# Optimization experiments

Measured on AMD Instinct MI355X. Metric: run time of the kernel, lower is better.

## Reference

```python
import jax, jax.numpy as jnp
import numpy as np

EPS = 1e-3  # denominator regularizer for weighted mean/cov
DIST_SCALE = 10.0  # raw_call applies 10.0 * distsq before exp weighting

V, K, C, F = 100000, 40, 3, 32


def setup_inputs() -> dict:
    key = jax.random.key(0)
    k1, k2, k3, k4 = jax.random.split(key, 4)
    coordinates = jax.random.normal(k1, (V, C), dtype=jnp.float32)
    distsq = jax.random.uniform(k2, (V, K), dtype=jnp.float32)  # squared distances >= 0
    features = jax.random.uniform(k3, (V, F), dtype=jnp.float32)  # non-negative activations
    n_idxs = jax.random.randint(k4, (V, K), 0, V, dtype=jnp.int32)
    return {"coordinates": coordinates, "distsq": distsq, "features": features, "n_idxs": n_idxs}


def reference(coordinates, distsq, features, n_idxs):
    nV, nC = coordinates.shape
    nF = features.shape[1]
    # SelectWithDefault semantics: index -1 -> default 0
    valid = (n_idxs >= 0)
    idx = jnp.where(valid, n_idxs, 0)
    n_coords = jnp.where(valid[..., None], coordinates[idx], 0.0)  # V x K x C
    w = jnp.exp(-DIST_SCALE * distsq)  # V x K distance weights
    n_feat = jnp.where(valid[..., None], features[idx], 0.0) * w[..., None]  # V x K x F (feature weights)
    wsum = jnp.sum(n_feat, axis=1)  # V x F
    denom = wsum[:, :, None] + EPS  # V x F x 1
    # weighted first moment -> means, weighted second moment -> covariance
    means = jnp.einsum('vkf,vkc->vfc', n_feat, n_coords) / denom  # V x F x C
    second = jnp.einsum('vkf,vkc,vkd->vfcd', n_feat, n_coords, n_coords) / denom[..., None]  # V x F x C x C
    cov = second - means[:, :, :, None] * means[:, :, None, :]  # centered covariance
    out = jnp.concatenate([cov.reshape(nV, nF * nC * nC), means.reshape(nV, nF * nC)], axis=-1)
    return out
```

## Files before the change

kernel.cpp:

```cpp
#include <hip/hip_runtime.h>


constexpr int K = 40;
constexpr int C = 3;
constexpr int F = 32;
constexpr float EPS = 1e-3f;
constexpr float DIST_SCALE = 10.0f;
constexpr int OUT_PER_V = F * C * C + F * C;
constexpr int VPB = 16;
constexpr int PAIRS = VPB * K;
constexpr int STAGE_F4 = VPB * 48;

typedef float    floatx4 __attribute__((ext_vector_type(4)));
typedef float    f32x8   __attribute__((ext_vector_type(8)));
typedef _Float16 f16x8   __attribute__((ext_vector_type(8)));

__global__ __launch_bounds__(256) void cvt_kernel(
    const float* __restrict__ in, _Float16* __restrict__ out16, int n8)
{
    const int i = blockIdx.x * 256 + threadIdx.x;
    if (i < n8) {
        const f32x8 v = __builtin_nontemporal_load((const f32x8*)in + i);
        const f16x8 o = __builtin_convertvector(v, f16x8);
        *((f16x8*)out16 + i) = o;
    }
}

template <typename FT>
__global__ __launch_bounds__(256) void neighcov_kernel(
    const float* __restrict__ coords,
    const float* __restrict__ distsq,
    const FT*    __restrict__ features,
    const int*   __restrict__ nidx,
    float* __restrict__ out,
    int V)
{
    __shared__ float4  s_wxyz[PAIRS];
    __shared__ int     s_joff[PAIRS];
    __shared__ floatx4 s_stage[STAGE_F4];

    const int tid   = threadIdx.x;
    const int vbase = blockIdx.x * VPB;
    const long long total_pairs = (long long)V * K;

    #pragma unroll
    for (int p = tid; p < PAIRS; p += 256) {
        const long long gp = (long long)vbase * K + p;
        int idx = -1;
        float d = 0.f;
        if (gp < total_pairs) {
            idx = __builtin_nontemporal_load(nidx + gp);
            d   = __builtin_nontemporal_load(distsq + gp);
        }
        const bool valid = (idx >= 0);
        const int j = valid ? idx : 0;
        const float w = valid ? __expf(-DIST_SCALE * d) : 0.f;
        const float x = coords[(size_t)j * 3 + 0];
        const float y = coords[(size_t)j * 3 + 1];
        const float z = coords[(size_t)j * 3 + 2];
        s_wxyz[p] = make_float4(w, x, y, z);
        s_joff[p] = j * F;
    }
    __syncthreads();

    const int fl   = tid & 15;
    const int vloc = tid >> 4;
    const float4* wp = &s_wxyz[vloc * K];
    const int*    jp = &s_joff[vloc * K];
    const int rem_v = V - vbase;
    floatx4* o4 = (floatx4*)(out + (size_t)vbase * OUT_PER_V);

    #pragma unroll
    for (int half = 0; half < 2; ++half) {
        const int f = half * 16 + fl;

        float wsum = 0.f;
        float m0 = 0.f, m1 = 0.f, m2 = 0.f;
        float s00 = 0.f, s01 = 0.f, s02 = 0.f, s11 = 0.f, s12 = 0.f, s22 = 0.f;

        #pragma unroll 8
        for (int k = 0; k < K; ++k) {
            const float4 q = wp[k];
            const int jo   = jp[k];
            const float feat = (float)features[jo + f];
            const float fw = q.x * feat;
            const float x = q.y, y = q.z, z = q.w;
            const float fx = fw * x, fy = fw * y, fz = fw * z;
            wsum += fw;
            m0 += fx;        m1 += fy;        m2 += fz;
            s00 += fx * x;   s01 += fx * y;   s02 += fx * z;
            s11 += fy * y;   s12 += fy * z;   s22 += fz * z;
        }

        const float inv = 1.f / (wsum + EPS);
        const float mu0 = m0 * inv, mu1 = m1 * inv, mu2 = m2 * inv;
        const float c00 = s00 * inv - mu0 * mu0;
        const float c01 = s01 * inv - mu0 * mu1;
        const float c02 = s02 * inv - mu0 * mu2;
        const float c11 = s11 * inv - mu1 * mu1;
        const float c12 = s12 * inv - mu1 * mu2;
        const float c22 = s22 * inv - mu2 * mu2;

        float* s_out = (float*)s_stage;
        float* so = s_out + vloc * 192 + fl * 9;
        so[0] = c00; so[1] = c01; so[2] = c02;
        so[3] = c01; so[4] = c11; so[5] = c12;
        so[6] = c02; so[7] = c12; so[8] = c22;
        float* sm = s_out + vloc * 192 + 144 + fl * 3;
        sm[0] = mu0; sm[1] = mu1; sm[2] = mu2;

        __syncthreads();

        #pragma unroll
        for (int g = tid; g < STAGE_F4; g += 256) {
            const int v = g / 48;
            const int r = g - v * 48;
            if (v < rem_v) {
                const int dst = v * 96 + (r < 36 ? half * 36 + r
                                                 : 72 + half * 12 + (r - 36));
                __builtin_nontemporal_store(s_stage[g], o4 + dst);
            }
        }

        __syncthreads();
    }
}

extern "C" void kernel_launch(void* const* d_in, const int* in_sizes, int n_in,
                              void* d_out, int out_size, void* d_ws, size_t ws_size,
                              hipStream_t stream) {
    const float* coords   = (const float*)d_in[0];
    const float* distsq   = (const float*)d_in[1];
    const float* features = (const float*)d_in[2];
    const int*   nidx     = (const int*)d_in[3];
    float* out = (float*)d_out;

    const int V = in_sizes[0] / C;
    const int blocks = (V + VPB - 1) / VPB;

    const size_t need = (size_t)V * F * sizeof(_Float16);
    const int nelem = V * F;
    if (ws_size >= need && (nelem & 7) == 0) {
        _Float16* feat16 = (_Float16*)d_ws;
        const int n8 = nelem / 8;
        cvt_kernel<<<(n8 + 255) / 256, 256, 0, stream>>>(features, feat16, n8);
        neighcov_kernel<_Float16><<<blocks, 256, 0, stream>>>(
            coords, distsq, feat16, nidx, out, V);
    } else {
        neighcov_kernel<float><<<blocks, 256, 0, stream>>>(
            coords, distsq, features, nidx, out, V);
    }
}
```

Measured before the change: 271.7 us.

## Split fp16 features into low/high half planes and pad shared weight array

The conversion kernel now writes features into two separate fp16 planes, one per 16-feature half. Each half-pass of the main kernel gathers from a compact 32-byte row instead of part of a 64-byte row, which aims to improve cache-line use for the random neighbor gathers. The shared weight/coordinate array is padded to stride K+1 to change the bank mapping, and the fp32 fallback is rewritten with 8 vertices per block. The trade-off is that each neighbor row is now touched twice, in two different planes, across the two passes.

```diff
diff --git a/kernel.cpp b/kernel.cpp
--- a/kernel.cpp
+++ b/kernel.cpp
@@ -4,11 +4,13 @@
 constexpr int K = 40;
 constexpr int C = 3;
 constexpr int F = 32;
+constexpr int FH = 16;
 constexpr float EPS = 1e-3f;
 constexpr float DIST_SCALE = 10.0f;
 constexpr int OUT_PER_V = F * C * C + F * C;
 constexpr int VPB = 16;
 constexpr int PAIRS = VPB * K;
+constexpr int WSTRIDE = K + 1;
 constexpr int STAGE_F4 = VPB * 48;
 
 typedef float    floatx4 __attribute__((ext_vector_type(4)));
@@ -16,26 +18,28 @@
 typedef _Float16 f16x8   __attribute__((ext_vector_type(8)));
 
 __global__ __launch_bounds__(256) void cvt_kernel(
-    const float* __restrict__ in, _Float16* __restrict__ out16, int n8)
+    const float* __restrict__ in, _Float16* __restrict__ lo,
+    _Float16* __restrict__ hi, int n4)
 {
     const int i = blockIdx.x * 256 + threadIdx.x;
-    if (i < n8) {
-        const f32x8 v = __builtin_nontemporal_load((const f32x8*)in + i);
-        const f16x8 o = __builtin_convertvector(v, f16x8);
-        *((f16x8*)out16 + i) = o;
-    }
-}
-
-template <typename FT>
-__global__ __launch_bounds__(256) void neighcov_kernel(
+    if (i >= n4) return;
+    const int v = i >> 2, q = i & 3;
+    const f32x8 x = __builtin_nontemporal_load((const f32x8*)in + i);
+    const f16x8 o = __builtin_convertvector(x, f16x8);
+    _Float16* dst = (q < 2 ? lo : hi) + (size_t)v * FH + (q & 1) * 8;
+    *(f16x8*)dst = o;
+}
+
+__global__ __launch_bounds__(256) void neighcov_split(
     const float* __restrict__ coords,
     const float* __restrict__ distsq,
-    const FT*    __restrict__ features,
+    const _Float16* __restrict__ plane_lo,
+    const _Float16* __restrict__ plane_hi,
     const int*   __restrict__ nidx,
     float* __restrict__ out,
     int V)
 {
-    __shared__ float4  s_wxyz[PAIRS];
+    __shared__ float4  s_wxyz[VPB * WSTRIDE];
     __shared__ int     s_joff[PAIRS];
     __shared__ floatx4 s_stage[STAGE_F4];
 
@@ -43,7 +47,6 @@
     const int vbase = blockIdx.x * VPB;
     const long long total_pairs = (long long)V * K;
 
-    #pragma unroll
     for (int p = tid; p < PAIRS; p += 256) {
         const long long gp = (long long)vbase * K + p;
         int idx = -1;
@@ -58,21 +61,22 @@
         const float x = coords[(size_t)j * 3 + 0];
         const float y = coords[(size_t)j * 3 + 1];
         const float z = coords[(size_t)j * 3 + 2];
-        s_wxyz[p] = make_float4(w, x, y, z);
-        s_joff[p] = j * F;
+        const int vloc = p / K, k = p - vloc * K;
+        s_wxyz[vloc * WSTRIDE + k] = make_float4(w, x, y, z);
+        s_joff[p] = j * FH;
     }
     __syncthreads();
 
     const int fl   = tid & 15;
     const int vloc = tid >> 4;
-    const float4* wp = &s_wxyz[vloc * K];
+    const float4* wp = &s_wxyz[vloc * WSTRIDE];
     const int*    jp = &s_joff[vloc * K];
     const int rem_v = V - vbase;
     floatx4* o4 = (floatx4*)(out + (size_t)vbase * OUT_PER_V);
 
     #pragma unroll
     for (int half = 0; half < 2; ++half) {
-        const int f = half * 16 + fl;
+        const _Float16* __restrict__ plane = half ? plane_hi : plane_lo;
 
         float wsum = 0.f;
         float m0 = 0.f, m1 = 0.f, m2 = 0.f;
@@ -82,7 +86,7 @@
         for (int k = 0; k < K; ++k) {
             const float4 q = wp[k];
             const int jo   = jp[k];
-            const float feat = (float)features[jo + f];
+            const float feat = (float)plane[jo + fl];
             const float fw = q.x * feat;
             const float x = q.y, y = q.z, z = q.w;
             const float fx = fw * x, fy = fw * y, fz = fw * z;
@@ -126,6 +130,77 @@
     }
 }
 
+constexpr int VPB8 = 8;
+constexpr int PAIRS8 = VPB8 * K;
+constexpr int OUT_F4_8 = VPB8 * OUT_PER_V / 4;
+
+__global__ __launch_bounds__(256) void neighcov_f32(
+    const float* __restrict__ coords, const float* __restrict__ distsq,
+    const float* __restrict__ features, const int* __restrict__ nidx,
+    float* __restrict__ out, int V)
+{
+    __shared__ float4  s_wxyz[PAIRS8];
+    __shared__ int     s_joff[PAIRS8];
+    __shared__ floatx4 s_out4[OUT_F4_8];
+
+    const int tid   = threadIdx.x;
+    const int vbase = blockIdx.x * VPB8;
+    const long long total_pairs = (long long)V * K;
+
+    #pragma unroll
+    for (int p = tid; p < PAIRS8; p += 256) {
+        const long long gp = (long long)vbase * K + p;
+        int idx = -1; float d = 0.f;
+        if (gp < total_pairs) {
+            idx = __builtin_nontemporal_load(nidx + gp);
+            d   = __builtin_nontemporal_load(distsq + gp);
+        }
+        const bool valid = (idx >= 0);
+        const int j = valid ? idx : 0;
+        const float w = valid ? __expf(-DIST_SCALE * d) : 0.f;
+        s_wxyz[p] = make_float4(w, coords[(size_t)j * 3 + 0],
+                                coords[(size_t)j * 3 + 1], coords[(size_t)j * 3 + 2]);
+        s_joff[p] = j * F;
+    }
+    __syncthreads();
+
+    const int f = tid & (F - 1), vloc = tid >> 5;
+    const float4* wp = &s_wxyz[vloc * K];
+    const int*    jp = &s_joff[vloc * K];
+
+    float wsum = 0.f, m0 = 0.f, m1 = 0.f, m2 = 0.f;
+    float s00 = 0.f, s01 = 0.f, s02 = 0.f, s11 = 0.f, s12 = 0.f, s22 = 0.f;
+    #pragma unroll 8
+    for (int k = 0; k < K; ++k) {
+        const float4 q = wp[k];
+        const float feat = features[jp[k] + f];
+        const float fw = q.x * feat;
+        const float x = q.y, y = q.z, z = q.w;
+        const float fx = fw * x, fy = fw * y, fz = fw * z;
+        wsum += fw; m0 += fx; m1 += fy; m2 += fz;
+        s00 += fx * x; s01 += fx * y; s02 += fx * z;
+        s11 += fy * y; s12 += fy * z; s22 += fz * z;
+    }
+    const float inv = 1.f / (wsum + EPS);
+    const float mu0 = m0 * inv, mu1 = m1 * inv, mu2 = m2 * inv;
+    float* s_out = (float*)s_out4;
+    float* so = s_out + vloc * OUT_PER_V + f * 9;
+    so[0] = s00 * inv - mu0 * mu0; so[1] = s01 * inv - mu0 * mu1;
+    so[2] = s02 * inv - mu0 * mu2; so[3] = so[1];
+    so[4] = s11 * inv - mu1 * mu1; so[5] = s12 * inv - mu1 * mu2;
+    so[6] = so[2]; so[7] = so[5]; so[8] = s22 * inv - mu2 * mu2;
+    float* sm = s_out + vloc * OUT_PER_V + F * 9 + f * 3;
+    sm[0] = mu0; sm[1] = mu1; sm[2] = mu2;
+    __syncthreads();
+
+    const int rem_v = V - vbase;
+    const int lim_f4 = (rem_v >= VPB8) ? OUT_F4_8 : rem_v * (OUT_PER_V / 4);
+    floatx4* o4 = (floatx4*)(out + (size_t)vbase * OUT_PER_V);
+    #pragma unroll
+    for (int g = tid; g < OUT_F4_8; g += 256)
+        if (g < lim_f4) __builtin_nontemporal_store(s_out4[g], o4 + g);
+}
+
 extern "C" void kernel_launch(void* const* d_in, const int* in_sizes, int n_in,
                               void* d_out, int out_size, void* d_ws, size_t ws_size,
                               hipStream_t stream) {
@@ -136,18 +211,19 @@
     float* out = (float*)d_out;
 
     const int V = in_sizes[0] / C;
-    const int blocks = (V + VPB - 1) / VPB;
-
-    const size_t need = (size_t)V * F * sizeof(_Float16);
-    const int nelem = V * F;
-    if (ws_size >= need && (nelem & 7) == 0) {
-        _Float16* feat16 = (_Float16*)d_ws;
-        const int n8 = nelem / 8;
-        cvt_kernel<<<(n8 + 255) / 256, 256, 0, stream>>>(features, feat16, n8);
-        neighcov_kernel<_Float16><<<blocks, 256, 0, stream>>>(
-            coords, distsq, feat16, nidx, out, V);
+
+    const size_t plane_bytes = (size_t)V * FH * sizeof(_Float16);
+    if (ws_size >= 2 * plane_bytes) {
+        _Float16* lo = (_Float16*)d_ws;
+        _Float16* hi = lo + (size_t)V * FH;
+        const int n4 = V * 4;
+        cvt_kernel<<<(n4 + 255) / 256, 256, 0, stream>>>(features, lo, hi, n4);
+        const int blocks = (V + VPB - 1) / VPB;
+        neighcov_split<<<blocks, 256, 0, stream>>>(
+            coords, distsq, lo, hi, nidx, out, V);
     } else {
-        neighcov_kernel<float><<<blocks, 256, 0, stream>>>(
+        const int blocks = (V + VPB8 - 1) / VPB8;
+        neighcov_f32<<<blocks, 256, 0, stream>>>(
             coords, distsq, features, nidx, out, V);
     }
 }
```

Measured after the change: 271.6 us. About the same (-0.0%).
